# Optimization experiments

Hardware: AMD Instinct MI355X
Metric: run time of the kernel (lower is better)

Reference implementation:

```python
import jax, jax.numpy as jnp
import numpy as np

N_FEATURES = 60
WINDOW = 64
N_FFT_BINS = WINDOW // 2 + 1  # 33
HIDDEN = 256
N_OUT = 3
TOTAL_IN = N_FEATURES + N_FEATURES * N_FFT_BINS  # 2040


def setup_inputs() -> dict:
    key = jax.random.key(0)
    ks = jax.random.split(key, 9)
    B, T = 4, 4096
    x = jax.random.normal(ks[0], (B, T, N_FEATURES), dtype=jnp.float32)

    def lin(k, fan_in, fan_out):
        bound = 1.0 / np.sqrt(fan_in)
        kw, kb = jax.random.split(k)
        W = jax.random.uniform(kw, (fan_in, fan_out), minval=-bound, maxval=bound, dtype=jnp.float32)
        b = jax.random.uniform(kb, (fan_out,), minval=-bound, maxval=bound, dtype=jnp.float32)
        return W, b

    W1, b1 = lin(ks[1], TOTAL_IN, HIDDEN)
    W2, b2 = lin(ks[2], HIDDEN, HIDDEN)
    W3, b3 = lin(ks[3], HIDDEN, HIDDEN // 2)
    W4, b4 = lin(ks[4], HIDDEN // 2, N_OUT)
    return {"x": x, "W1": W1, "b1": b1, "W2": W2, "b2": b2,
            "W3": W3, "b3": b3, "W4": W4, "b4": b4}


def _fft_features(x):
    # x: [B, T, F]
    B, T, F = x.shape
    half_w = WINDOW // 2
    # reflect pad along time: (half_w, half_w - 1)
    xp = jnp.pad(x, ((0, 0), (half_w, half_w - 1), (0, 0)), mode='reflect')  # [B, T+W-1, F]
    # sliding windows: [B, T, W, F] -> [B, T, F, W] (matches torch unfold layout)
    idx = jnp.arange(T)[:, None] + jnp.arange(WINDOW)[None, :]  # [T, W]
    windows = xp[:, idx, :].transpose(0, 1, 3, 2)  # [B, T, F, W]
    fft_mag = jnp.log1p(jnp.abs(jnp.fft.rfft(windows, axis=-1)))  # [B, T, F, W//2+1]
    return fft_mag.reshape(B, T, F * N_FFT_BINS)


def reference(x, W1, b1, W2, b2, W3, b3, W4, b4):
    fft_flat = _fft_features(x)
    h = jnp.concatenate([x, fft_flat], axis=-1)  # [B, T, 2040]
    h = jax.nn.relu(h @ W1 + b1)   # dropout is identity in eval mode
    h = jax.nn.relu(h @ W2 + b2)
    h = jax.nn.relu(h @ W3 + b3)
    return h @ W4 + b4             # [B, T, 3]
```

## Files before the change

kernel.cpp:

```cpp
#include <hip/hip_runtime.h>
#include <math.h>

#define T_LEN 4096
#define NF 60
#define NBINS 33
#define KPAD 2048
#define HID 256
#define NTOK 16384
#define LINE 4208

typedef _Float16 half_t;
typedef half_t half8 __attribute__((ext_vector_type(8)));
typedef half_t half4 __attribute__((ext_vector_type(4)));
typedef float f32x4 __attribute__((ext_vector_type(4)));

constexpr double K_PI = 3.14159265358979323846;
constexpr double tcos(double x) {
    while (x >  K_PI) x -= 2.0 * K_PI;
    while (x < -K_PI) x += 2.0 * K_PI;
    double x2 = x * x, s = 0.0, term = 1.0;
    for (int m = 0; m < 14; ++m) { s += term; term *= -x2 / ((2.0*m + 1.0) * (2.0*m + 2.0)); }
    return s;
}
struct CosTab { float v[64]; };
constexpr CosTab make_tab() {
    CosTab t{};
    for (int j = 0; j < 64; ++j) t.v[j] = (float)tcos(2.0 * K_PI * (double)j / 64.0);
    return t;
}
__device__ constexpr CosTab CTd = make_tab();

__device__ __forceinline__ float log2_1p(float x) {
    return __log2f(1.0f + x);
}

__global__ __launch_bounds__(256) void prep_kernel(
        const float* __restrict__ W1, const float* __restrict__ W2,
        const float* __restrict__ W3,
        half_t* __restrict__ dftH,
        half_t* __restrict__ W1T, half_t* __restrict__ W2T,
        half_t* __restrict__ W3T) {
    int i = blockIdx.x * 256 + threadIdx.x;
    if (i < 4096) {
        int row = i >> 6, n = i & 63;
        float c = (row < 33) ? CTd.v[(row * n) & 63]
                             : CTd.v[((row - 32) * n + 48) & 63];
        dftH[i] = (half_t)c;
        return;
    }
    i -= 4096;
    if (i < 256 * KPAD) {
        int gk = i & (KPAD - 1);
        float v = 0.f;
        if (gk < 2040) {
            int j = i >> 11;
            int r;
            bool isfft = true;
            if (gk < 1920) {
                int f = gk >> 5, bin = gk & 31;
                r = NF + f * NBINS + bin;
            } else if (gk < 1980) {
                r = gk - 1920; isfft = false;
            } else {
                r = NF + (gk - 1980) * NBINS + 32;
            }
            v = W1[(size_t)r * HID + j];
            if (isfft) v *= 0.69314718055994531f;
        }
        W1T[i] = (half_t)v;
        return;
    }
    i -= 256 * KPAD;
    if (i < 256 * 256) {
        int k = i & 255, j = i >> 8;
        W2T[i] = (half_t)W2[(size_t)k * HID + j];
        return;
    }
    i -= 256 * 256;
    if (i < 128 * 256) {
        int k = i & 255, j = i >> 8;
        W3T[i] = (half_t)W3[(size_t)k * 128 + j];
    }
}

__global__ __launch_bounds__(256) void xr_kernel(
        const float* __restrict__ x, half_t* __restrict__ lineG,
        half_t* __restrict__ H0) {
    if (blockIdx.x < 240) {
        const int bf = blockIdx.x;
        const int b = bf / NF, f = bf - b * NF;
        const float* xb = x + (size_t)b * T_LEN * NF + f;
        half_t* L = lineG + (size_t)bf * LINE;
        for (int j = threadIdx.x; j < LINE; j += 256) {
            int s = j - 32;
            int r = (s < 0) ? -s : ((s > T_LEN - 1) ? 2 * (T_LEN - 1) - s : s);
            L[j] = (half_t)xb[(size_t)r * NF];
        }
        return;
    }
    const int t = (blockIdx.x - 240) * 256 + threadIdx.x;
    const int b = t >> 12, tl = t & (T_LEN - 1);
    const int i = (b << 12) + ((tl & 7) << 9) + (tl >> 3);
    const float* xp = x + (size_t)t * NF;
    half_t* hp = H0 + (size_t)i * KPAD;
#pragma unroll
    for (int f4 = 0; f4 < 15; ++f4) {
        float4 v = *(const float4*)(xp + f4 * 4);
        half4 h;
        h[0] = (half_t)v.x; h[1] = (half_t)v.y;
        h[2] = (half_t)v.z; h[3] = (half_t)v.w;
        *(half4*)&hp[1920 + f4 * 4] = h;
    }
    half8 z = {};
    *(half8*)&hp[2040] = z;
}

__global__ __launch_bounds__(256) void fft_hankel(
        const half_t* __restrict__ lineG, const half_t* __restrict__ dftH,
        half_t* __restrict__ H0) {
    __shared__ half_t L[4160];
    __shared__ half_t Tt[4][16 * 36];

    const int bid = blockIdx.x;
    const int bf = bid >> 3, c = bid & 7;
    const int b = bf / NF, f = bf - b * NF;
    const int tid = threadIdx.x;
    const int lane = tid & 63, wv = tid >> 6;
    const int lr = lane & 15, lg = lane >> 4;

    half8 a[4][2];
#pragma unroll
    for (int rf = 0; rf < 4; ++rf)
#pragma unroll
        for (int ks = 0; ks < 2; ++ks)
            a[rf][ks] = *(const half8*)&dftH[(16 * rf + lr) * 64 + ks * 32 + lg * 8];

    {
        const half_t* src = lineG + (size_t)bf * LINE + c;
        for (int j = tid; j < 4152; j += 256) L[j] = src[j];
    }
    __syncthreads();

    const int i0 = (b << 12) + (c << 9);
    const int sl = wv * 128 + lr;
    const int tl = lane >> 2, q = lane & 3;

    half8 w0 = *(const half8*)&L[8 * sl + lg * 8];
    half8 w1 = *(const half8*)&L[8 * sl + 32 + lg * 8];

#pragma unroll
    for (int cs = 0; cs < 8; ++cs) {
        f32x4 dacc[4] = {};
#pragma unroll
        for (int rf = 0; rf < 4; ++rf)
            dacc[rf] = __builtin_amdgcn_mfma_f32_16x16x32_f16(a[rf][0], w0, dacc[rf], 0, 0, 0);
#pragma unroll
        for (int rf = 0; rf < 4; ++rf)
            dacc[rf] = __builtin_amdgcn_mfma_f32_16x16x32_f16(a[rf][1], w1, dacc[rf], 0, 0, 0);

        if (cs < 7) {
            const int sn = sl + (cs + 1) * 16;
            w0 = *(const half8*)&L[8 * sn + lg * 8];
            w1 = *(const half8*)&L[8 * sn + 32 + lg * 8];
        }

#pragma unroll
        for (int rf = 0; rf < 2; ++rf) {
            half4 h4;
#pragma unroll
            for (int r = 0; r < 4; ++r) {
                float re = dacc[rf][r];
                float im = dacc[rf + 2][r];
                float v = (rf == 0 && r == 0)
                    ? ((lg == 0) ? log2_1p(fabsf(re))
                                 : log2_1p(sqrtf(re * re + im * im)))
                    : log2_1p(sqrtf(re * re + im * im));
                h4[r] = (half_t)v;
            }
            *(half4*)&Tt[wv][lr * 36 + rf * 16 + lg * 4] = h4;
        }
        asm volatile("s_waitcnt lgkmcnt(0)" ::: "memory");
        {
            half8 rowv = *(const half8*)&Tt[wv][tl * 36 + q * 8];
            const int gtok = i0 + wv * 128 + cs * 16 + tl;
            *(half8*)&H0[(size_t)gtok * KPAD + f * 32 + q * 8] = rowv;
        }
        if (lg == 0)
            H0[(size_t)(i0 + sl + cs * 16) * KPAD + 1980 + f] =
                (half_t)log2_1p(fabsf(dacc[2][0]));
    }
}

template<int BN>
__global__ __launch_bounds__(256, 2) void gemm_pipe(
        const half_t* __restrict__ A, int lda,
        const half_t* __restrict__ BT, int ldb,
        const float* __restrict__ bias,
        half_t* __restrict__ Ch, int N, int K) {
    constexpr int NFR = BN / 64;
    __shared__ half_t As[2][64 * 64];

    const int tid  = threadIdx.x;
    const int row0 = blockIdx.x * 64;
    const int col0 = blockIdx.y * BN;
    const int wv = tid >> 6, lane = tid & 63;
    const int lr = lane & 15, lg = lane >> 4;

    const int srow = tid >> 2, sg = (tid & 3) * 2;
    const int wo0 = srow * 64 + ((sg ^ (srow & 7)) * 8);
    const int wo1 = srow * 64 + (((sg + 1) ^ (srow & 7)) * 8);
    const half_t* ap = A + (size_t)(row0 + srow) * lda + sg * 8;

    const half_t* bp[NFR];
#pragma unroll
    for (int nf = 0; nf < NFR; ++nf)
        bp[nf] = BT + (size_t)(col0 + wv * (16 * NFR) + nf * 16 + lr) * ldb + lg * 8;

    f32x4 acc[4][NFR] = {};
    const int NIT = K / 64;

    half8 bcur[2][NFR], bnxt[2][NFR];
    half8 pa0, pa1, pb0, pb1;

    {
        half8 v0 = *(const half8*)(ap);
        half8 v1 = *(const half8*)(ap + 8);
        *(half8*)&As[0][wo0] = v0;
        *(half8*)&As[0][wo1] = v1;
    }
    if (NIT > 1) { pa0 = *(const half8*)(ap + 64);  pa1 = *(const half8*)(ap + 72); }
    if (NIT > 2) { pb0 = *(const half8*)(ap + 128); pb1 = *(const half8*)(ap + 136); }
#pragma unroll
    for (int ks = 0; ks < 2; ++ks)
#pragma unroll
        for (int nf = 0; nf < NFR; ++nf)
            bcur[ks][nf] = *(const half8*)(bp[nf] + ks * 32);

    for (int it = 0; it < NIT; it += 2) {
        __syncthreads();
        if (it + 1 < NIT) {
#pragma unroll
            for (int ks = 0; ks < 2; ++ks)
#pragma unroll
                for (int nf = 0; nf < NFR; ++nf)
                    bnxt[ks][nf] = *(const half8*)(bp[nf] + (it + 1) * 64 + ks * 32);
        }
#pragma unroll
        for (int ks = 0; ks < 2; ++ks) {
            half8 af[4];
#pragma unroll
            for (int mf = 0; mf < 4; ++mf)
                af[mf] = *(const half8*)&As[0][(mf * 16 + lr) * 64 + (((ks * 4 + lg) ^ (lr & 7)) * 8)];
#pragma unroll
            for (int mf = 0; mf < 4; ++mf)
#pragma unroll
                for (int nf = 0; nf < NFR; ++nf)
                    acc[mf][nf] = __builtin_amdgcn_mfma_f32_16x16x32_f16(af[mf], bcur[ks][nf], acc[mf][nf], 0, 0, 0);
        }
        if (it + 1 < NIT) { *(half8*)&As[1][wo0] = pa0; *(half8*)&As[1][wo1] = pa1; }
        if (it + 3 < NIT) { pa0 = *(const half8*)(ap + (it + 3) * 64); pa1 = *(const half8*)(ap + (it + 3) * 64 + 8); }
        if (it + 1 >= NIT) break;

        __syncthreads();
        if (it + 2 < NIT) {
#pragma unroll
            for (int ks = 0; ks < 2; ++ks)
#pragma unroll
                for (int nf = 0; nf < NFR; ++nf)
                    bcur[ks][nf] = *(const half8*)(bp[nf] + (it + 2) * 64 + ks * 32);
        }
#pragma unroll
        for (int ks = 0; ks < 2; ++ks) {
            half8 af[4];
#pragma unroll
            for (int mf = 0; mf < 4; ++mf)
                af[mf] = *(const half8*)&As[1][(mf * 16 + lr) * 64 + (((ks * 4 + lg) ^ (lr & 7)) * 8)];
#pragma unroll
            for (int mf = 0; mf < 4; ++mf)
#pragma unroll
                for (int nf = 0; nf < NFR; ++nf)
                    acc[mf][nf] = __builtin_amdgcn_mfma_f32_16x16x32_f16(af[mf], bnxt[ks][nf], acc[mf][nf], 0, 0, 0);
        }
        if (it + 2 < NIT) { *(half8*)&As[0][wo0] = pb0; *(half8*)&As[0][wo1] = pb1; }
        if (it + 4 < NIT) { pb0 = *(const half8*)(ap + (it + 4) * 64); pb1 = *(const half8*)(ap + (it + 4) * 64 + 8); }
    }

#pragma unroll
    for (int nf = 0; nf < NFR; ++nf) {
        int col = col0 + wv * (16 * NFR) + nf * 16 + lr;
        float bs = bias[col];
#pragma unroll
        for (int mf = 0; mf < 4; ++mf)
#pragma unroll
            for (int r = 0; r < 4; ++r) {
                int row = row0 + mf * 16 + lg * 4 + r;
                Ch[(size_t)row * N + col] = (half_t)fmaxf(acc[mf][nf][r] + bs, 0.f);
            }
    }
}

__global__ __launch_bounds__(256) void gemm3_head(
        const half_t* __restrict__ A, const half_t* __restrict__ BT,
        const float* __restrict__ b3, const float* __restrict__ W4,
        const float* __restrict__ b4, float* __restrict__ out) {
    constexpr int NFR = 2, NIT = 4;
    __shared__ half_t As[2][64 * 64];
    __shared__ float Hs[64][132];
    __shared__ float W4s[384];

    const int tid  = threadIdx.x;
    const int row0 = blockIdx.x * 64;
    const int wv = tid >> 6, lane = tid & 63;
    const int lr = lane & 15, lg = lane >> 4;

    for (int i = tid; i < 384; i += 256) W4s[i] = W4[i];

    const int srow = tid >> 2, sg = (tid & 3) * 2;
    const int wo0 = srow * 64 + ((sg ^ (srow & 7)) * 8);
    const int wo1 = srow * 64 + (((sg + 1) ^ (srow & 7)) * 8);
    const half_t* ap = A + (size_t)(row0 + srow) * 256 + sg * 8;

    const half_t* bp[NFR];
#pragma unroll
    for (int nf = 0; nf < NFR; ++nf)
        bp[nf] = BT + (size_t)(wv * 32 + nf * 16 + lr) * 256 + lg * 8;

    f32x4 acc[4][NFR] = {};
    half8 bcur[2][NFR], bnxt[2][NFR];
    half8 pa0, pa1, pb0, pb1;

    {
        half8 v0 = *(const half8*)(ap);
        half8 v1 = *(const half8*)(ap + 8);
        *(half8*)&As[0][wo0] = v0;
        *(half8*)&As[0][wo1] = v1;
    }
    pa0 = *(const half8*)(ap + 64);  pa1 = *(const half8*)(ap + 72);
    pb0 = *(const half8*)(ap + 128); pb1 = *(const half8*)(ap + 136);
#pragma unroll
    for (int ks = 0; ks < 2; ++ks)
#pragma unroll
        for (int nf = 0; nf < NFR; ++nf)
            bcur[ks][nf] = *(const half8*)(bp[nf] + ks * 32);

    for (int it = 0; it < NIT; it += 2) {
        __syncthreads();
        if (it + 1 < NIT) {
#pragma unroll
            for (int ks = 0; ks < 2; ++ks)
#pragma unroll
                for (int nf = 0; nf < NFR; ++nf)
                    bnxt[ks][nf] = *(const half8*)(bp[nf] + (it + 1) * 64 + ks * 32);
        }
#pragma unroll
        for (int ks = 0; ks < 2; ++ks) {
            half8 af[4];
#pragma unroll
            for (int mf = 0; mf < 4; ++mf)
                af[mf] = *(const half8*)&As[0][(mf * 16 + lr) * 64 + (((ks * 4 + lg) ^ (lr & 7)) * 8)];
#pragma unroll
            for (int mf = 0; mf < 4; ++mf)
#pragma unroll
                for (int nf = 0; nf < NFR; ++nf)
                    acc[mf][nf] = __builtin_amdgcn_mfma_f32_16x16x32_f16(af[mf], bcur[ks][nf], acc[mf][nf], 0, 0, 0);
        }
        if (it + 1 < NIT) { *(half8*)&As[1][wo0] = pa0; *(half8*)&As[1][wo1] = pa1; }
        if (it + 3 < NIT) { pa0 = *(const half8*)(ap + (it + 3) * 64); pa1 = *(const half8*)(ap + (it + 3) * 64 + 8); }
        if (it + 1 >= NIT) break;

        __syncthreads();
        if (it + 2 < NIT) {
#pragma unroll
            for (int ks = 0; ks < 2; ++ks)
#pragma unroll
                for (int nf = 0; nf < NFR; ++nf)
                    bcur[ks][nf] = *(const half8*)(bp[nf] + (it + 2) * 64 + ks * 32);
        }
#pragma unroll
        for (int ks = 0; ks < 2; ++ks) {
            half8 af[4];
#pragma unroll
            for (int mf = 0; mf < 4; ++mf)
                af[mf] = *(const half8*)&As[1][(mf * 16 + lr) * 64 + (((ks * 4 + lg) ^ (lr & 7)) * 8)];
#pragma unroll
            for (int mf = 0; mf < 4; ++mf)
#pragma unroll
                for (int nf = 0; nf < NFR; ++nf)
                    acc[mf][nf] = __builtin_amdgcn_mfma_f32_16x16x32_f16(af[mf], bnxt[ks][nf], acc[mf][nf], 0, 0, 0);
        }
        if (it + 2 < NIT) { *(half8*)&As[0][wo0] = pb0; *(half8*)&As[0][wo1] = pb1; }
        if (it + 4 < NIT) { pb0 = *(const half8*)(ap + (it + 4) * 64); pb1 = *(const half8*)(ap + (it + 4) * 64 + 8); }
    }

#pragma unroll
    for (int nf = 0; nf < NFR; ++nf) {
        int col = wv * 32 + nf * 16 + lr;
        float bs = b3[col];
#pragma unroll
        for (int mf = 0; mf < 4; ++mf)
#pragma unroll
            for (int r = 0; r < 4; ++r)
                Hs[mf * 16 + lg * 4 + r][col] = fmaxf(acc[mf][nf][r] + bs, 0.f);
    }
    __syncthreads();

    const int row = tid >> 2, q = tid & 3;
    float a0 = 0.f, a1 = 0.f, a2 = 0.f;
#pragma unroll
    for (int k = 0; k < 32; ++k) {
        float hv = Hs[row][q * 32 + k];
        a0 = fmaf(hv, W4s[(q * 32 + k) * 3 + 0], a0);
        a1 = fmaf(hv, W4s[(q * 32 + k) * 3 + 1], a1);
        a2 = fmaf(hv, W4s[(q * 32 + k) * 3 + 2], a2);
    }
    a0 += __shfl_xor(a0, 1); a0 += __shfl_xor(a0, 2);
    a1 += __shfl_xor(a1, 1); a1 += __shfl_xor(a1, 2);
    a2 += __shfl_xor(a2, 1); a2 += __shfl_xor(a2, 2);
    if (q == 0) {
        const int i = row0 + row;
        const int b = i >> 12, c = (i >> 9) & 7, s = i & 511;
        const int t = (b << 12) + (s << 3) + c;
        float* o = out + (size_t)t * 3;
        o[0] = a0 + b4[0]; o[1] = a1 + b4[1]; o[2] = a2 + b4[2];
    }
}

extern "C" void kernel_launch(void* const* d_in, const int* in_sizes, int n_in,
                              void* d_out, int out_size, void* d_ws, size_t ws_size,
                              hipStream_t stream) {
    (void)in_sizes; (void)n_in; (void)out_size; (void)ws_size;
    const float* x  = (const float*)d_in[0];
    const float* W1 = (const float*)d_in[1];
    const float* b1 = (const float*)d_in[2];
    const float* W2 = (const float*)d_in[3];
    const float* b2 = (const float*)d_in[4];
    const float* W3 = (const float*)d_in[5];
    const float* b3 = (const float*)d_in[6];
    const float* W4 = (const float*)d_in[7];
    const float* b4 = (const float*)d_in[8];
    float* out = (float*)d_out;

    char* w = (char*)d_ws;
    half_t* H0    = (half_t*)(w);
    half_t* H1    = (half_t*)(w + (size_t)64 * 1024 * 1024);
    half_t* H2    = (half_t*)(w + (size_t)72 * 1024 * 1024);
    half_t* W1T   = (half_t*)(w + (size_t)88 * 1024 * 1024);
    half_t* W2T   = (half_t*)(w + (size_t)89 * 1024 * 1024);
    half_t* W3T   = W2T + 256 * 256;
    half_t* dftH  = W3T + 128 * 256;
    half_t* lineG = (half_t*)(w + (size_t)90 * 1024 * 1024);

    prep_kernel<<<2448, 256, 0, stream>>>(W1, W2, W3, dftH, W1T, W2T, W3T);
    xr_kernel<<<304, 256, 0, stream>>>(x, lineG, H0);
    fft_hankel<<<240 * 8, 256, 0, stream>>>(lineG, dftH, H0);

    gemm_pipe<128><<<dim3(NTOK / 64, 2), 256, 0, stream>>>(
        H0, KPAD, W1T, KPAD, b1, H1, HID, KPAD);
    gemm_pipe<128><<<dim3(NTOK / 64, 2), 256, 0, stream>>>(
        H1, HID, W2T, HID, b2, H2, HID, HID);
    gemm3_head<<<NTOK / 64, 256, 0, stream>>>(H2, W3T, b3, W4, b4, out);
}
```

Baseline: 101.9 us.

## Enlarge GEMM block tile to 128x128 with 2x2 warp layout

Replaces the 64x128 templated GEMM with a 128x128 tile kernel where the four waves form a 2x2 grid, each computing a 64x64 sub-tile from a shared A tile. This halves the number of blocks and doubles per-wave MFMA work per A/B fragment load, so each B fragment loaded from global memory is reused across more rows. In exchange, LDS use doubles, register pressure rises (16 accumulators plus larger prefetch buffers), the launch-bounds occupancy hint is dropped, and only 256 blocks launch for the two big GEMMs, which may underfill the GPU's compute units.

Result: slower. 114.7 us (+12.5%).

```diff
diff --git a/kernel.cpp b/kernel.cpp
--- a/kernel.cpp
+++ b/kernel.cpp
@@ -191,49 +191,60 @@
     }
 }
 
-template<int BN>
-__global__ __launch_bounds__(256, 2) void gemm_pipe(
+__global__ __launch_bounds__(256) void gemm_big(
         const half_t* __restrict__ A, int lda,
         const half_t* __restrict__ BT, int ldb,
         const float* __restrict__ bias,
         half_t* __restrict__ Ch, int N, int K) {
-    constexpr int NFR = BN / 64;
-    __shared__ half_t As[2][64 * 64];
+    __shared__ half_t As[2][128 * 64];
 
     const int tid  = threadIdx.x;
-    const int row0 = blockIdx.x * 64;
-    const int col0 = blockIdx.y * BN;
+    const int row0 = blockIdx.x * 128;
+    const int col0 = blockIdx.y * 128;
     const int wv = tid >> 6, lane = tid & 63;
     const int lr = lane & 15, lg = lane >> 4;
-
-    const int srow = tid >> 2, sg = (tid & 3) * 2;
-    const int wo0 = srow * 64 + ((sg ^ (srow & 7)) * 8);
-    const int wo1 = srow * 64 + (((sg + 1) ^ (srow & 7)) * 8);
+    const int wr = wv >> 1, wc = wv & 1;
+
+    const int srow = tid >> 1, sg = (tid & 1) * 4;
+    int wo[4];
+#pragma unroll
+    for (int i = 0; i < 4; ++i)
+        wo[i] = srow * 64 + (((sg + i) ^ (srow & 7)) * 8);
     const half_t* ap = A + (size_t)(row0 + srow) * lda + sg * 8;
 
-    const half_t* bp[NFR];
-#pragma unroll
-    for (int nf = 0; nf < NFR; ++nf)
-        bp[nf] = BT + (size_t)(col0 + wv * (16 * NFR) + nf * 16 + lr) * ldb + lg * 8;
-
-    f32x4 acc[4][NFR] = {};
+    const half_t* bp[4];
+#pragma unroll
+    for (int nf = 0; nf < 4; ++nf)
+        bp[nf] = BT + (size_t)(col0 + wc * 64 + nf * 16 + lr) * ldb + lg * 8;
+
+    f32x4 acc[4][4] = {};
     const int NIT = K / 64;
 
-    half8 bcur[2][NFR], bnxt[2][NFR];
-    half8 pa0, pa1, pb0, pb1;
+    half8 bcur[2][4], bnxt[2][4];
+    half8 pa[4], pb[4];
 
     {
         half8 v0 = *(const half8*)(ap);
         half8 v1 = *(const half8*)(ap + 8);
-        *(half8*)&As[0][wo0] = v0;
-        *(half8*)&As[0][wo1] = v1;
-    }
-    if (NIT > 1) { pa0 = *(const half8*)(ap + 64);  pa1 = *(const half8*)(ap + 72); }
-    if (NIT > 2) { pb0 = *(const half8*)(ap + 128); pb1 = *(const half8*)(ap + 136); }
+        half8 v2 = *(const half8*)(ap + 16);
+        half8 v3 = *(const half8*)(ap + 24);
+        *(half8*)&As[0][wo[0]] = v0;
+        *(half8*)&As[0][wo[1]] = v1;
+        *(half8*)&As[0][wo[2]] = v2;
+        *(half8*)&As[0][wo[3]] = v3;
+    }
+    if (NIT > 1) {
+#pragma unroll
+        for (int i = 0; i < 4; ++i) pa[i] = *(const half8*)(ap + 64 + i * 8);
+    }
+    if (NIT > 2) {
+#pragma unroll
+        for (int i = 0; i < 4; ++i) pb[i] = *(const half8*)(ap + 128 + i * 8);
+    }
 #pragma unroll
     for (int ks = 0; ks < 2; ++ks)
 #pragma unroll
-        for (int nf = 0; nf < NFR; ++nf)
+        for (int nf = 0; nf < 4; ++nf)
             bcur[ks][nf] = *(const half8*)(bp[nf] + ks * 32);
 
     for (int it = 0; it < NIT; it += 2) {
@@ -242,7 +253,7 @@
 #pragma unroll
             for (int ks = 0; ks < 2; ++ks)
 #pragma unroll
-                for (int nf = 0; nf < NFR; ++nf)
+                for (int nf = 0; nf < 4; ++nf)
                     bnxt[ks][nf] = *(const half8*)(bp[nf] + (it + 1) * 64 + ks * 32);
         }
 #pragma unroll
@@ -250,15 +261,21 @@
             half8 af[4];
 #pragma unroll
             for (int mf = 0; mf < 4; ++mf)
-                af[mf] = *(const half8*)&As[0][(mf * 16 + lr) * 64 + (((ks * 4 + lg) ^ (lr & 7)) * 8)];
-#pragma unroll
-            for (int mf = 0; mf < 4; ++mf)
-#pragma unroll
-                for (int nf = 0; nf < NFR; ++nf)
+                af[mf] = *(const half8*)&As[0][(wr * 64 + mf * 16 + lr) * 64 + (((ks * 4 + lg) ^ (lr & 7)) * 8)];
+#pragma unroll
+            for (int mf = 0; mf < 4; ++mf)
+#pragma unroll
+                for (int nf = 0; nf < 4; ++nf)
                     acc[mf][nf] = __builtin_amdgcn_mfma_f32_16x16x32_f16(af[mf], bcur[ks][nf], acc[mf][nf], 0, 0, 0);
         }
-        if (it + 1 < NIT) { *(half8*)&As[1][wo0] = pa0; *(half8*)&As[1][wo1] = pa1; }
-        if (it + 3 < NIT) { pa0 = *(const half8*)(ap + (it + 3) * 64); pa1 = *(const half8*)(ap + (it + 3) * 64 + 8); }
+        if (it + 1 < NIT) {
+#pragma unroll
+            for (int i = 0; i < 4; ++i) *(half8*)&As[1][wo[i]] = pa[i];
+        }
+        if (it + 3 < NIT) {
+#pragma unroll
+            for (int i = 0; i < 4; ++i) pa[i] = *(const half8*)(ap + (it + 3) * 64 + i * 8);
+        }
         if (it + 1 >= NIT) break;
 
         __syncthreads();
@@ -266,7 +283,7 @@
 #pragma unroll
             for (int ks = 0; ks < 2; ++ks)
 #pragma unroll
-                for (int nf = 0; nf < NFR; ++nf)
+                for (int nf = 0; nf < 4; ++nf)
                     bcur[ks][nf] = *(const half8*)(bp[nf] + (it + 2) * 64 + ks * 32);
         }
 #pragma unroll
@@ -274,26 +291,32 @@
             half8 af[4];
 #pragma unroll
             for (int mf = 0; mf < 4; ++mf)
-                af[mf] = *(const half8*)&As[1][(mf * 16 + lr) * 64 + (((ks * 4 + lg) ^ (lr & 7)) * 8)];
-#pragma unroll
-            for (int mf = 0; mf < 4; ++mf)
-#pragma unroll
-                for (int nf = 0; nf < NFR; ++nf)
+                af[mf] = *(const half8*)&As[1][(wr * 64 + mf * 16 + lr) * 64 + (((ks * 4 + lg) ^ (lr & 7)) * 8)];
+#pragma unroll
+            for (int mf = 0; mf < 4; ++mf)
+#pragma unroll
+                for (int nf = 0; nf < 4; ++nf)
                     acc[mf][nf] = __builtin_amdgcn_mfma_f32_16x16x32_f16(af[mf], bnxt[ks][nf], acc[mf][nf], 0, 0, 0);
         }
-        if (it + 2 < NIT) { *(half8*)&As[0][wo0] = pb0; *(half8*)&As[0][wo1] = pb1; }
-        if (it + 4 < NIT) { pb0 = *(const half8*)(ap + (it + 4) * 64); pb1 = *(const half8*)(ap + (it + 4) * 64 + 8); }
-    }
-
-#pragma unroll
-    for (int nf = 0; nf < NFR; ++nf) {
-        int col = col0 + wv * (16 * NFR) + nf * 16 + lr;
+        if (it + 2 < NIT) {
+#pragma unroll
+            for (int i = 0; i < 4; ++i) *(half8*)&As[0][wo[i]] = pb[i];
+        }
+        if (it + 4 < NIT) {
+#pragma unroll
+            for (int i = 0; i < 4; ++i) pb[i] = *(const half8*)(ap + (it + 4) * 64 + i * 8);
+        }
+    }
+
+#pragma unroll
+    for (int nf = 0; nf < 4; ++nf) {
+        int col = col0 + wc * 64 + nf * 16 + lr;
         float bs = bias[col];
 #pragma unroll
         for (int mf = 0; mf < 4; ++mf)
 #pragma unroll
             for (int r = 0; r < 4; ++r) {
-                int row = row0 + mf * 16 + lg * 4 + r;
+                int row = row0 + wr * 64 + mf * 16 + lg * 4 + r;
                 Ch[(size_t)row * N + col] = (half_t)fmaxf(acc[mf][nf][r] + bs, 0.f);
             }
     }
@@ -454,9 +477,9 @@
     xr_kernel<<<304, 256, 0, stream>>>(x, lineG, H0);
     fft_hankel<<<240 * 8, 256, 0, stream>>>(lineG, dftH, H0);
 
-    gemm_pipe<128><<<dim3(NTOK / 64, 2), 256, 0, stream>>>(
+    gemm_big<<<dim3(NTOK / 128, 2), 256, 0, stream>>>(
         H0, KPAD, W1T, KPAD, b1, H1, HID, KPAD);
-    gemm_pipe<128><<<dim3(NTOK / 64, 2), 256, 0, stream>>>(
+    gemm_big<<<dim3(NTOK / 128, 2), 256, 0, stream>>>(
         H1, HID, W2T, HID, b2, H2, HID, HID);
     gemm3_head<<<NTOK / 64, 256, 0, stream>>>(H2, W3T, b3, W4, b4, out);
 }
```

## Replace register-staged double-buffered A tile with direct global-to-LDS loads

Applied to the files above, without the earlier changes.

The GEMM kernel now fills the A tile through global_load_lds (buffer loads written directly into shared memory) into a single LDS buffer, rather than a register-staged, double-buffered pipeline with prefetch two iterations ahead. The loop becomes one iteration per K-chunk, with a barrier before and after compute and B fragments loaded each iteration. This frees registers and LDS and simplifies the loop, but it drops the overlap of global loads with MFMA compute, so load latency may be exposed at every step.

After: 105.2 us. +3.2%, slower.

```diff
diff --git a/kernel.cpp b/kernel.cpp
--- a/kernel.cpp
+++ b/kernel.cpp
@@ -13,6 +13,12 @@
 typedef half_t half8 __attribute__((ext_vector_type(8)));
 typedef half_t half4 __attribute__((ext_vector_type(4)));
 typedef float f32x4 __attribute__((ext_vector_type(4)));
+
+__device__ __forceinline__ void gload16(const half_t* g, half_t* l) {
+    __builtin_amdgcn_global_load_lds(
+        (const __attribute__((address_space(1))) void*)g,
+        (__attribute__((address_space(3))) void*)l, 16, 0, 0);
+}
 
 constexpr double K_PI = 3.14159265358979323846;
 constexpr double tcos(double x) {
@@ -192,13 +198,13 @@
 }
 
 template<int BN>
-__global__ __launch_bounds__(256, 2) void gemm_pipe(
+__global__ __launch_bounds__(256, 2) void gemm_m97(
         const half_t* __restrict__ A, int lda,
         const half_t* __restrict__ BT, int ldb,
         const float* __restrict__ bias,
         half_t* __restrict__ Ch, int N, int K) {
     constexpr int NFR = BN / 64;
-    __shared__ half_t As[2][64 * 64];
+    __shared__ half_t As[64 * 64];
 
     const int tid  = threadIdx.x;
     const int row0 = blockIdx.x * 64;
@@ -206,10 +212,12 @@
     const int wv = tid >> 6, lane = tid & 63;
     const int lr = lane & 15, lg = lane >> 4;
 
-    const int srow = tid >> 2, sg = (tid & 3) * 2;
-    const int wo0 = srow * 64 + ((sg ^ (srow & 7)) * 8);
-    const int wo1 = srow * 64 + (((sg + 1) ^ (srow & 7)) * 8);
-    const half_t* ap = A + (size_t)(row0 + srow) * lda + sg * 8;
+    const int arow = (lane >> 3);
+    const int agr  = (lane & 7) ^ arow;
+    const half_t* apg0 = A + (size_t)(row0 + wv * 16 + arow) * lda + agr * 8;
+    const half_t* apg1 = apg0 + (size_t)8 * lda;
+    half_t* l0 = &As[(wv * 16) * 64];
+    half_t* l1 = &As[(wv * 16 + 8) * 64];
 
     const half_t* bp[NFR];
 #pragma unroll
@@ -219,70 +227,32 @@
     f32x4 acc[4][NFR] = {};
     const int NIT = K / 64;
 
-    half8 bcur[2][NFR], bnxt[2][NFR];
-    half8 pa0, pa1, pb0, pb1;
-
-    {
-        half8 v0 = *(const half8*)(ap);
-        half8 v1 = *(const half8*)(ap + 8);
-        *(half8*)&As[0][wo0] = v0;
-        *(half8*)&As[0][wo1] = v1;
-    }
-    if (NIT > 1) { pa0 = *(const half8*)(ap + 64);  pa1 = *(const half8*)(ap + 72); }
-    if (NIT > 2) { pb0 = *(const half8*)(ap + 128); pb1 = *(const half8*)(ap + 136); }
-#pragma unroll
-    for (int ks = 0; ks < 2; ++ks)
-#pragma unroll
-        for (int nf = 0; nf < NFR; ++nf)
-            bcur[ks][nf] = *(const half8*)(bp[nf] + ks * 32);
-
-    for (int it = 0; it < NIT; it += 2) {
+    for (int it = 0; it < NIT; ++it) {
+        gload16(apg0 + it * 64, l0);
+        gload16(apg1 + it * 64, l1);
+        half8 bf[2][NFR];
+#pragma unroll
+        for (int ks = 0; ks < 2; ++ks)
+#pragma unroll
+            for (int nf = 0; nf < NFR; ++nf)
+                bf[ks][nf] = *(const half8*)(bp[nf] + it * 64 + ks * 32);
+
         __syncthreads();
-        if (it + 1 < NIT) {
-#pragma unroll
-            for (int ks = 0; ks < 2; ++ks)
-#pragma unroll
-                for (int nf = 0; nf < NFR; ++nf)
-                    bnxt[ks][nf] = *(const half8*)(bp[nf] + (it + 1) * 64 + ks * 32);
-        }
+
 #pragma unroll
         for (int ks = 0; ks < 2; ++ks) {
             half8 af[4];
 #pragma unroll
             for (int mf = 0; mf < 4; ++mf)
-                af[mf] = *(const half8*)&As[0][(mf * 16 + lr) * 64 + (((ks * 4 + lg) ^ (lr & 7)) * 8)];
+                af[mf] = *(const half8*)&As[(mf * 16 + lr) * 64 + (((ks * 4 + lg) ^ (lr & 7)) * 8)];
 #pragma unroll
             for (int mf = 0; mf < 4; ++mf)
 #pragma unroll
                 for (int nf = 0; nf < NFR; ++nf)
-                    acc[mf][nf] = __builtin_amdgcn_mfma_f32_16x16x32_f16(af[mf], bcur[ks][nf], acc[mf][nf], 0, 0, 0);
-        }
-        if (it + 1 < NIT) { *(half8*)&As[1][wo0] = pa0; *(half8*)&As[1][wo1] = pa1; }
-        if (it + 3 < NIT) { pa0 = *(const half8*)(ap + (it + 3) * 64); pa1 = *(const half8*)(ap + (it + 3) * 64 + 8); }
-        if (it + 1 >= NIT) break;
+                    acc[mf][nf] = __builtin_amdgcn_mfma_f32_16x16x32_f16(af[mf], bf[ks][nf], acc[mf][nf], 0, 0, 0);
+        }
 
         __syncthreads();
-        if (it + 2 < NIT) {
-#pragma unroll
-            for (int ks = 0; ks < 2; ++ks)
-#pragma unroll
-                for (int nf = 0; nf < NFR; ++nf)
-                    bcur[ks][nf] = *(const half8*)(bp[nf] + (it + 2) * 64 + ks * 32);
-        }
-#pragma unroll
-        for (int ks = 0; ks < 2; ++ks) {
-            half8 af[4];
-#pragma unroll
-            for (int mf = 0; mf < 4; ++mf)
-                af[mf] = *(const half8*)&As[1][(mf * 16 + lr) * 64 + (((ks * 4 + lg) ^ (lr & 7)) * 8)];
-#pragma unroll
-            for (int mf = 0; mf < 4; ++mf)
-#pragma unroll
-                for (int nf = 0; nf < NFR; ++nf)
-                    acc[mf][nf] = __builtin_amdgcn_mfma_f32_16x16x32_f16(af[mf], bnxt[ks][nf], acc[mf][nf], 0, 0, 0);
-        }
-        if (it + 2 < NIT) { *(half8*)&As[0][wo0] = pb0; *(half8*)&As[0][wo1] = pb1; }
-        if (it + 4 < NIT) { pb0 = *(const half8*)(ap + (it + 4) * 64); pb1 = *(const half8*)(ap + (it + 4) * 64 + 8); }
     }
 
 #pragma unroll
@@ -454,9 +424,9 @@
     xr_kernel<<<304, 256, 0, stream>>>(x, lineG, H0);
     fft_hankel<<<240 * 8, 256, 0, stream>>>(lineG, dftH, H0);
 
-    gemm_pipe<128><<<dim3(NTOK / 64, 2), 256, 0, stream>>>(
+    gemm_m97<128><<<dim3(NTOK / 64, 2), 256, 0, stream>>>(
         H0, KPAD, W1T, KPAD, b1, H1, HID, KPAD);
-    gemm_pipe<128><<<dim3(NTOK / 64, 2), 256, 0, stream>>>(
+    gemm_m97<128><<<dim3(NTOK / 64, 2), 256, 0, stream>>>(
         H1, HID, W2T, HID, b2, H2, HID, HID);
     gemm3_head<<<NTOK / 64, 256, 0, stream>>>(H2, W3T, b3, W4, b4, out);
 }
```
